# Performance work log

Hardware: AMD Instinct MI355X
Metric: run time of the kernel (lower is better)

## Reference

```python
import jax, jax.numpy as jnp
import numpy as np

DENSITY = 985.0  # kg/m^3, body density used by BodyMeasurements for mass
EPS = 1e-12


def _measure(v_shaped, faces_tensor, circ_vert_idx, height_vert_idx):
    # Gather triangles: [B, F, 3(verts), 3(xyz)]
    tris = v_shaped[:, faces_tensor]
    v0, v1, v2 = tris[:, :, 0, :], tris[:, :, 1, :], tris[:, :, 2, :]

    # --- mass: signed tetrahedron volumes summed over faces ---
    vol = jnp.einsum('bfi,bfi->b', v0, jnp.cross(v1, v2)) / 6.0
    mass = jnp.abs(vol) * DENSITY                       # [B]

    # --- height: vertical distance between two landmark vertices ---
    height = jnp.abs(v_shaped[:, height_vert_idx[0], 1]
                     - v_shaped[:, height_vert_idx[1], 1])  # [B]

    # --- circumferences: horizontal plane y = y(landmark) intersected with mesh ---
    plane_y = v_shaped[:, circ_vert_idx, 1]             # [B, M] per-batch plane heights
    pa = tris                                           # edge starts  [B,F,3,3]
    pb = jnp.roll(tris, -1, axis=2)                     # edge ends    [B,F,3,3]
    ya = pa[..., 1]                                     # [B,F,3]
    yb = pb[..., 1]
    py = plane_y[:, None, None, :]                      # [B,1,1,M]
    da = ya[..., None] - py                             # signed dist of edge start [B,F,3,M]
    db = yb[..., None] - py
    crossing = (da * db) < 0.0                          # edge straddles plane
    t = da / jnp.where(crossing, da - db, 1.0)          # safe param along edge
    # intersection points on the plane: [B,F,3(edges),M,3]
    pts = pa[..., None, :] + t[..., None] * (pb - pa)[..., None, :]
    # a crossing triangle has exactly 2 crossing edges -> one active edge pair
    pts_n = jnp.roll(pts, -1, axis=2)
    pair_ok = crossing & jnp.roll(crossing, -1, axis=2)  # [B,F,3,M]
    d = jnp.where(pair_ok[..., None], pts_n - pts, 0.0)
    seg_len = jnp.sqrt(jnp.sum(d * d, axis=-1) + EPS) * pair_ok  # [B,F,3,M]
    circ = jnp.sum(seg_len, axis=(1, 2))                # [B, M]

    # mass, height, chest, waist, hips -> [B, 5]
    return jnp.concatenate([mass[:, None], height[:, None], circ], axis=1)


def setup_inputs() -> dict:
    key = jax.random.key(0)
    k1, k2, k3, k4 = jax.random.split(key, 4)
    B, V, F = 256, 6890, 13776
    v_shaped = jax.random.normal(k1, (B, V, 3), dtype=jnp.float32)
    faces_tensor = jax.random.randint(k2, (F, 3), 0, V)
    circ_vert_idx = jax.random.randint(k3, (3,), 0, V)
    height_vert_idx = jax.random.randint(k4, (2,), 0, V)
    return {
        'v_shaped': v_shaped,
        'faces_tensor': faces_tensor,
        'circ_vert_idx': circ_vert_idx,
        'height_vert_idx': height_vert_idx,
    }


def reference(v_shaped, faces_tensor, circ_vert_idx, height_vert_idx):
    return _measure(v_shaped, faces_tensor, circ_vert_idx, height_vert_idx)
```

## Files before the change

kernel.cpp:

```cpp
#include <hip/hip_runtime.h>
#include <math.h>

#define NV      6890
#define BLOCK   1024
#define NWAVES  (BLOCK / 64)
#define DENSITY 985.0f

typedef float v2f __attribute__((ext_vector_type(2)));

__device__ __forceinline__ float frcp(float x)  { return __builtin_amdgcn_rcpf(x); }
__device__ __forceinline__ float fsqrt(float x) { return __builtin_amdgcn_sqrtf(x); }

__device__ __forceinline__ unsigned bf16rtn_hi(float f) {
    return (__float_as_uint(f) + 0x8000u) & 0xffff0000u;
}
__device__ __forceinline__ unsigned bf16rtn_lo(float f) {
    return (__float_as_uint(f) + 0x8000u) >> 16;
}

__global__ __launch_bounds__(BLOCK) void measure_kernel(
    const float* __restrict__ v,
    const int*   __restrict__ faces,
    const int*   __restrict__ circ_idx,
    const int*   __restrict__ h_idx,
    float*       __restrict__ out,
    int F)
{
    extern __shared__ float lds[];
    uint2* vslot = reinterpret_cast<uint2*>(lds);
    float* red   = lds + 2 * NV;

    const int b = blockIdx.x;
    const float* vb = v + (size_t)b * NV * 3;

    {
        const v2f* vb2 = reinterpret_cast<const v2f*>(vb);
        const int NSLOT = NV / 2;
        for (int j = threadIdx.x; j < NSLOT; j += BLOCK) {
            const v2f a = vb2[3 * j + 0];
            const v2f m = vb2[3 * j + 1];
            const v2f c = vb2[3 * j + 2];
            const unsigned p0 = bf16rtn_hi(a.x) | bf16rtn_lo(m.x);
            const unsigned p1 = bf16rtn_hi(m.y) | bf16rtn_lo(c.y);
            vslot[2 * j + 0] = make_uint2(__float_as_uint(a.y), p0);
            vslot[2 * j + 1] = make_uint2(__float_as_uint(c.x), p1);
        }
    }
    __syncthreads();

    const float pys[3] = { __uint_as_float(vslot[circ_idx[0]].x),
                           __uint_as_float(vslot[circ_idx[1]].x),
                           __uint_as_float(vslot[circ_idx[2]].x) };

    float vol = 0.0f;
    float circ[3] = {0.0f, 0.0f, 0.0f};

    #pragma unroll 2
    for (int f = threadIdx.x; f < F; f += BLOCK) {
        const int i0 = faces[3 * f + 0];
        const int i1 = faces[3 * f + 1];
        const int i2 = faces[3 * f + 2];

        const uint2 s0 = vslot[i0];
        const uint2 s1 = vslot[i1];
        const uint2 s2 = vslot[i2];
        const float y0 = __uint_as_float(s0.x);
        const float y1 = __uint_as_float(s1.x);
        const float y2 = __uint_as_float(s2.x);
        const v2f xz0 = { __uint_as_float(s0.y & 0xffff0000u), __uint_as_float(s0.y << 16) };
        const v2f xz1 = { __uint_as_float(s1.y & 0xffff0000u), __uint_as_float(s1.y << 16) };
        const v2f xz2 = { __uint_as_float(s2.y & 0xffff0000u), __uint_as_float(s2.y << 16) };

        {
            const float cx = y1 * xz2.y - xz1.y * y2;
            const float cy = xz1.y * xz2.x - xz1.x * xz2.y;
            const float cz = xz1.x * y2 - y1 * xz2.x;
            vol += xz0.x * cx + y0 * cy + xz0.y * cz;
        }

        const v2f g01 = (xz1 - xz0) * frcp(y0 - y1);
        const v2f g12 = (xz2 - xz1) * frcp(y1 - y2);
        const v2f g20 = (xz0 - xz2) * frcp(y2 - y0);

        const v2f w0 = g01 - g20;
        const v2f w1 = g01 - g12;
        const v2f w2 = g12 - g20;
        const float h0 = fsqrt(fmaf(w0.x, w0.x, w0.y * w0.y));
        const float h1 = fsqrt(fmaf(w1.x, w1.x, w1.y * w1.y));
        const float h2 = fsqrt(fmaf(w2.x, w2.x, w2.y * w2.y));

        #pragma unroll
        for (int p = 0; p < 3; ++p) {
            const float py = pys[p];
            const bool b0 = y0 < py;
            const bool b1 = y1 < py;
            const bool b2 = y2 < py;
            const bool c0 = b0 != b1;
            const bool c1 = b1 != b2;
            const bool c2 = b2 != b0;

            const float d0 = y0 - py;
            const float d1 = y1 - py;
            const float d2 = y2 - py;

            float dsel = c2 ? d0 : d1;
            float hsel = c2 ? h0 : h1;
            dsel = c0 ? dsel : d2;
            hsel = c0 ? hsel : h2;
            const bool valid = c0 || c1 || c2;

            const float L = fabsf(dsel) * hsel;
            circ[p] += valid ? L : 0.0f;
        }
    }

    #pragma unroll
    for (int off = 32; off > 0; off >>= 1) {
        vol     += __shfl_down(vol,     off);
        circ[0] += __shfl_down(circ[0], off);
        circ[1] += __shfl_down(circ[1], off);
        circ[2] += __shfl_down(circ[2], off);
    }
    const int lane = threadIdx.x & 63;
    const int wid  = threadIdx.x >> 6;
    if (lane == 0) {
        red[wid * 4 + 0] = vol;
        red[wid * 4 + 1] = circ[0];
        red[wid * 4 + 2] = circ[1];
        red[wid * 4 + 3] = circ[2];
    }
    __syncthreads();

    const int tid = threadIdx.x;
    if (tid < 4) {
        float s = 0.0f;
        for (int w = 0; w < NWAVES; ++w) s += red[w * 4 + tid];
        if (tid == 0) out[b * 5 + 0] = fabsf(s / 6.0f) * DENSITY;
        else          out[b * 5 + 1 + tid] = s;
    } else if (tid == 4) {
        const float hy0 = __uint_as_float(vslot[h_idx[0]].x);
        const float hy1 = __uint_as_float(vslot[h_idx[1]].x);
        out[b * 5 + 1] = fabsf(hy0 - hy1);
    }
}

extern "C" void kernel_launch(void* const* d_in, const int* in_sizes, int n_in,
                              void* d_out, int out_size, void* d_ws, size_t ws_size,
                              hipStream_t stream) {
    const float* v        = (const float*)d_in[0];
    const int*   faces    = (const int*)d_in[1];
    const int*   circ_idx = (const int*)d_in[2];
    const int*   h_idx    = (const int*)d_in[3];
    float*       out      = (float*)d_out;

    const int B = in_sizes[0] / (NV * 3);
    const int F = in_sizes[1] / 3;

    const size_t lds_bytes = (size_t)(2 * NV + NWAVES * 4) * sizeof(float);
    measure_kernel<<<B, BLOCK, lds_bytes, stream>>>(v, faces, circ_idx, h_idx, out, F);
}
```

Measured before the change: 16.42 us.

## Split each batch's faces across two blocks with cross-block workspace handoff

```diff
diff --git a/kernel.cpp b/kernel.cpp
--- a/kernel.cpp
+++ b/kernel.cpp
@@ -5,6 +5,7 @@
 #define BLOCK   1024
 #define NWAVES  (BLOCK / 64)
 #define DENSITY 985.0f
+#define SENTINEL 0x5A5A7E3Du
 
 typedef float v2f __attribute__((ext_vector_type(2)));
 
@@ -18,19 +19,21 @@
     return (__float_as_uint(f) + 0x8000u) >> 16;
 }
 
-__global__ __launch_bounds__(BLOCK) void measure_kernel(
+__global__ __launch_bounds__(BLOCK, 8) void measure_kernel(
     const float* __restrict__ v,
     const int*   __restrict__ faces,
     const int*   __restrict__ circ_idx,
     const int*   __restrict__ h_idx,
     float*       __restrict__ out,
+    unsigned*    __restrict__ ws,
     int F)
 {
     extern __shared__ float lds[];
     uint2* vslot = reinterpret_cast<uint2*>(lds);
     float* red   = lds + 2 * NV;
 
-    const int b = blockIdx.x;
+    const int b = blockIdx.x >> 1;
+    const int h = blockIdx.x & 1;
     const float* vb = v + (size_t)b * NV * 3;
 
     {
@@ -55,8 +58,12 @@
     float vol = 0.0f;
     float circ[3] = {0.0f, 0.0f, 0.0f};
 
+    const int F2 = F >> 1;
+    const int lo = h ? F2 : 0;
+    const int hi = h ? F  : F2;
+
     #pragma unroll 2
-    for (int f = threadIdx.x; f < F; f += BLOCK) {
+    for (int f = lo + threadIdx.x; f < hi; f += BLOCK) {
         const int i0 = faces[3 * f + 0];
         const int i1 = faces[3 * f + 1];
         const int i2 = faces[3 * f + 2];
@@ -131,16 +138,45 @@
     }
     __syncthreads();
 
+    unsigned* wsb = ws + 8 * b;
     const int tid = threadIdx.x;
-    if (tid < 4) {
-        float s = 0.0f;
-        for (int w = 0; w < NWAVES; ++w) s += red[w * 4 + tid];
-        if (tid == 0) out[b * 5 + 0] = fabsf(s / 6.0f) * DENSITY;
-        else          out[b * 5 + 1 + tid] = s;
-    } else if (tid == 4) {
-        const float hy0 = __uint_as_float(vslot[h_idx[0]].x);
-        const float hy1 = __uint_as_float(vslot[h_idx[1]].x);
-        out[b * 5 + 1] = fabsf(hy0 - hy1);
+
+    if (h == 1) {
+        if (tid == 0) {
+            float s0 = 0.f, s1 = 0.f, s2 = 0.f, s3 = 0.f;
+            for (int w = 0; w < NWAVES; ++w) {
+                s0 += red[w * 4 + 0]; s1 += red[w * 4 + 1];
+                s2 += red[w * 4 + 2]; s3 += red[w * 4 + 3];
+            }
+            __hip_atomic_store(&wsb[0], __float_as_uint(s0), __ATOMIC_RELAXED, __HIP_MEMORY_SCOPE_AGENT);
+            __hip_atomic_store(&wsb[1], __float_as_uint(s1), __ATOMIC_RELAXED, __HIP_MEMORY_SCOPE_AGENT);
+            __hip_atomic_store(&wsb[2], __float_as_uint(s2), __ATOMIC_RELAXED, __HIP_MEMORY_SCOPE_AGENT);
+            __hip_atomic_store(&wsb[3], __float_as_uint(s3), __ATOMIC_RELAXED, __HIP_MEMORY_SCOPE_AGENT);
+            __hip_atomic_store(&wsb[4], SENTINEL, __ATOMIC_RELEASE, __HIP_MEMORY_SCOPE_AGENT);
+        }
+    } else {
+        if (tid == 0) {
+            float s0 = 0.f, s1 = 0.f, s2 = 0.f, s3 = 0.f;
+            for (int w = 0; w < NWAVES; ++w) {
+                s0 += red[w * 4 + 0]; s1 += red[w * 4 + 1];
+                s2 += red[w * 4 + 2]; s3 += red[w * 4 + 3];
+            }
+            int guard = 0;
+            while (__hip_atomic_load(&wsb[4], __ATOMIC_ACQUIRE, __HIP_MEMORY_SCOPE_AGENT) != SENTINEL
+                   && guard < (1 << 28)) ++guard;
+            s0 += __uint_as_float(__hip_atomic_load(&wsb[0], __ATOMIC_RELAXED, __HIP_MEMORY_SCOPE_AGENT));
+            s1 += __uint_as_float(__hip_atomic_load(&wsb[1], __ATOMIC_RELAXED, __HIP_MEMORY_SCOPE_AGENT));
+            s2 += __uint_as_float(__hip_atomic_load(&wsb[2], __ATOMIC_RELAXED, __HIP_MEMORY_SCOPE_AGENT));
+            s3 += __uint_as_float(__hip_atomic_load(&wsb[3], __ATOMIC_RELAXED, __HIP_MEMORY_SCOPE_AGENT));
+            out[b * 5 + 0] = fabsf(s0 / 6.0f) * DENSITY;
+            out[b * 5 + 2] = s1;
+            out[b * 5 + 3] = s2;
+            out[b * 5 + 4] = s3;
+        } else if (tid == 4) {
+            const float hy0 = __uint_as_float(vslot[h_idx[0]].x);
+            const float hy1 = __uint_as_float(vslot[h_idx[1]].x);
+            out[b * 5 + 1] = fabsf(hy0 - hy1);
+        }
     }
 }
 
@@ -152,10 +188,11 @@
     const int*   circ_idx = (const int*)d_in[2];
     const int*   h_idx    = (const int*)d_in[3];
     float*       out      = (float*)d_out;
+    unsigned*    ws       = (unsigned*)d_ws;
 
     const int B = in_sizes[0] / (NV * 3);
     const int F = in_sizes[1] / 3;
 
     const size_t lds_bytes = (size_t)(2 * NV + NWAVES * 4) * sizeof(float);
-    measure_kernel<<<B, BLOCK, lds_bytes, stream>>>(v, faces, circ_idx, h_idx, out, F);
+    measure_kernel<<<2 * B, BLOCK, lds_bytes, stream>>>(v, faces, circ_idx, h_idx, out, ws, F);
 }
```

Measured after the change: 24.12 us. 46.9% more time.
